# Kernel tuning notes

Hardware: AMD Instinct MI355X
Metric: run time of the kernel (lower is better)

Reference implementation:

```python
import jax, jax.numpy as jnp
import numpy as np

D_MODEL = 2048
D_INNER = 4096            # expand * d_model
D_XB = 1024
D_STATE = 128
HEADDIM = 64
NHEADS = D_INNER // HEADDIM            # 64
NGROUPS = D_INNER // D_STATE           # 32 (d_inner == ngroups * d_state)
HPG = NHEADS // NGROUPS                # heads per B/C group = 2
REPEAT = D_INNER // D_XB               # repeat_kv factor = 4
XB_GROUPS = D_XB // D_STATE            # 8
CHUNK = 256
D_CONV = 4
CONV_DIM = D_INNER + 2 * D_XB          # 6144
D_IN_PROJ = D_INNER + 2 * D_XB + D_INNER + NHEADS  # 10304 -> d_mlp = 0
NORM_GS = D_INNER // NGROUPS           # gated group-RMSNorm group size = 128
EPS = 1e-5


def setup_inputs() -> dict:
    key = jax.random.key(0)
    ks = jax.random.split(key, 8)
    u = jax.random.normal(ks[0], (2, 2048, D_MODEL), jnp.float32)
    W_in = jax.random.normal(ks[1], (D_IN_PROJ, D_MODEL), jnp.float32) * 0.02
    conv_w = jax.random.normal(ks[2], (CONV_DIM, D_CONV), jnp.float32) * 0.2
    conv_b = jnp.zeros((CONV_DIM,), jnp.float32)
    # dt_bias = inverse-softplus of dt ~ LogUniform(dt_min, dt_max), as in __init__
    dt = jnp.exp(jax.random.uniform(ks[3], (NHEADS,), jnp.float32)
                 * (np.log(0.1) - np.log(0.001)) + np.log(0.001))
    dt_bias = dt + jnp.log(-jnp.expm1(-dt))
    A_log = jnp.log(jax.random.uniform(ks[4], (NHEADS,), jnp.float32, minval=1.0, maxval=16.0))
    D = jnp.ones((NHEADS,), jnp.float32)
    norm_weight = jnp.ones((D_INNER,), jnp.float32)
    W_out = jax.random.normal(ks[5], (D_MODEL, D_INNER), jnp.float32) * 0.02
    return dict(u=u, W_in=W_in, conv_w=conv_w, conv_b=conv_b, dt_bias=dt_bias,
                A_log=A_log, D=D, norm_weight=norm_weight, W_out=W_out)


def _segsum(x):
    # x: (..., T); out[..., t, s] = sum_{s < i <= t} x_i for s <= t else -inf
    T = x.shape[-1]
    cs = jnp.cumsum(x, axis=-1)
    seg = cs[..., :, None] - cs[..., None, :]
    mask = jnp.tril(jnp.ones((T, T), bool))
    return jnp.where(mask, seg, -jnp.inf)


def _chunked_scan(x, dt, A, Bh, Ch, D):
    # SSD chunked selective scan (mamba_chunk_scan_combined math).
    # x: (b,l,h,p), dt: (b,l,h) post-softplus, A: (h,), Bh/Ch: (b,l,h,n), D: (h,)
    b, l, h, p = x.shape
    c = l // CHUNK
    xc = x.reshape(b, c, CHUNK, h, p)
    dtc = dt.reshape(b, c, CHUNK, h)
    Bc = Bh.reshape(b, c, CHUNK, h, D_STATE)
    Cc = Ch.reshape(b, c, CHUNK, h, D_STATE)
    dA = jnp.transpose(dtc * A, (0, 3, 1, 2))          # (b,h,c,cl)
    dA_cs = jnp.cumsum(dA, axis=-1)                     # (b,h,c,cl)
    L = jnp.exp(_segsum(dA))                            # (b,h,c,cl,cl), lower-tri decay
    xdt = xc * dtc[..., None]                           # (b,c,cl,h,p)
    # intra-chunk (diagonal block) output
    G = jnp.einsum('bclhn,bcshn->bhcls', Cc, Bc)
    Y_diag = jnp.einsum('bhcls,bcshp->bclhp', G * L, xdt)
    # per-chunk final states
    decay_states = jnp.exp(dA_cs[..., -1:] - dA_cs)     # (b,h,c,cl)
    states = jnp.einsum('bcshn,bhcs,bcshp->bchpn', Bc, decay_states, xdt)
    # inter-chunk recurrence
    chunk_decay = jnp.exp(dA_cs[..., -1])               # (b,h,c)
    states_t = jnp.moveaxis(states, 1, 0)               # (c,b,h,p,n)
    decay_t = jnp.moveaxis(chunk_decay, -1, 0)          # (c,b,h)
    def step(carry, inp):
        s, d = inp
        return carry * d[..., None, None] + s, carry
    _, prev = jax.lax.scan(step, jnp.zeros_like(states_t[0]), (states_t, decay_t))
    prev = jnp.moveaxis(prev, 0, 1)                     # (b,c,h,p,n) state entering each chunk
    Y_off = jnp.einsum('bclhn,bchpn,bhcl->bclhp', Cc, prev, jnp.exp(dA_cs))
    y = Y_diag + Y_off + xc * D[:, None]                # D skip uses raw x
    return y.reshape(b, l, h, p)


def reference(u, W_in, conv_w, conv_b, dt_bias, A_log, D, norm_weight, W_out):
    b, l, _ = u.shape
    zxbcdt = u @ W_in.T                                 # (b,l,10304); d_mlp == 0
    z, xBC, dt = jnp.split(zxbcdt, [D_INNER, D_INNER + CONV_DIM], axis=-1)
    # causal depthwise conv1d (kernel D_CONV) + SiLU (causal_conv1d_fn semantics)
    xp = jnp.pad(xBC, ((0, 0), (D_CONV - 1, 0), (0, 0)))
    conv = conv_b
    for k in range(D_CONV):
        conv = conv + xp[:, k:k + l, :] * conv_w[:, k]
    xBC = jax.nn.silu(conv)
    x, B, C = jnp.split(xBC, [D_XB, 2 * D_XB], axis=-1)
    # GQA-style repeat_kv (repeat_interleave over d_state-sized groups)
    x = jnp.repeat(x.reshape(b, l, XB_GROUPS, D_STATE), REPEAT, axis=2).reshape(b, l, D_INNER)
    B = jnp.repeat(B.reshape(b, l, XB_GROUPS, D_STATE), REPEAT, axis=2)   # (b,l,NGROUPS,n)
    C = C.reshape(b, l, NGROUPS, D_STATE)
    # broadcast groups to heads (head h uses group h // HPG)
    Bh = jnp.repeat(B, HPG, axis=2)
    Ch = jnp.repeat(C, HPG, axis=2)
    xh = x.reshape(b, l, NHEADS, HEADDIM)
    dt = jax.nn.softplus(dt + dt_bias)                  # dt_softplus=True
    A = -jnp.exp(A_log)
    y = _chunked_scan(xh, dt, A, Bh, Ch, D).reshape(b, l, D_INNER)
    # RMSNormGated (norm_before_gate=False): gate then grouped RMSNorm
    y = y * jax.nn.silu(z)
    yg = y.reshape(b, l, NGROUPS, NORM_GS)
    rstd = jax.lax.rsqrt(jnp.mean(yg * yg, axis=-1, keepdims=True) + EPS)
    y = (yg * rstd).reshape(b, l, D_INNER) * norm_weight
    return y @ W_out.T
```

## Files before the change

kernel.cpp:

```cpp
#include <hip/hip_runtime.h>
#include <cstdint>
#include <cstddef>

typedef unsigned int uint;
typedef unsigned short ushort;

typedef __bf16 bf16x8 __attribute__((ext_vector_type(8)));
typedef float f32x4 __attribute__((ext_vector_type(4)));

__device__ __forceinline__ float bflo(uint u) { return __uint_as_float(u << 16); }
__device__ __forceinline__ float bfhi(uint u) { return __uint_as_float(u & 0xffff0000u); }
__device__ __forceinline__ float bf2f(ushort s) { return __uint_as_float(((uint)s) << 16); }
__device__ __forceinline__ ushort f2bf(float f) {
    uint u = __float_as_uint(f);
    u += 0x7fffu + ((u >> 16) & 1u);
    return (ushort)(u >> 16);
}
__device__ __forceinline__ uint pk2(float lo, float hi) {
    return (uint)f2bf(lo) | ((uint)f2bf(hi) << 16);
}
__device__ __forceinline__ void unpack8(uint4 v, float* f) {
    f[0] = bflo(v.x); f[1] = bfhi(v.x); f[2] = bflo(v.y); f[3] = bfhi(v.y);
    f[4] = bflo(v.z); f[5] = bfhi(v.z); f[6] = bflo(v.w); f[7] = bfhi(v.w);
}

typedef __attribute__((address_space(1))) const unsigned int* as1_cuptr;
typedef __attribute__((address_space(3))) unsigned int* as3_uptr;
__device__ __forceinline__ void gload_lds16(const void* g, void* l) {
    __builtin_amdgcn_global_load_lds((as1_cuptr)g, (as3_uptr)l, 16, 0, 0);
}

#define LTOT 4096
#define DMODEL 2048
#define DINNER 4096
#define DSTATE 128
#define NHEADS 64
#define CONVDIM 6144
#define DPROJ 10304
#define CHUNK 256
#define NCHUNK 16

__global__ void cvt_all(const float* __restrict__ u, const float* __restrict__ Wi,
                        const float* __restrict__ Wo, ushort* __restrict__ ub,
                        ushort* __restrict__ wib, ushort* __restrict__ wob) {
    int i = blockIdx.x * 256 + threadIdx.x;
    const float* src; ushort* dst; int j;
    if (i < 2097152)      { src = u;  dst = ub;  j = i; }
    else if (i < 7372800) { src = Wi; dst = wib; j = i - 2097152; }
    else if (i < 9469952) { src = Wo; dst = wob; j = i - 7372800; }
    else return;
    float4 v = ((const float4*)src)[j];
    ushort4 o;
    o.x = f2bf(v.x); o.y = f2bf(v.y); o.z = f2bf(v.z); o.w = f2bf(v.w);
    ((ushort4*)dst)[j] = o;
}

#define MFMA_OP __builtin_amdgcn_mfma_f32_16x16x32_bf16
#define MMX(MB, AV, BV) do { \
  _Pragma("unroll") \
  for (int _m = 0; _m < 4; _m++) \
    _Pragma("unroll") \
    for (int _n = 0; _n < 4; _n++) \
      acc[(MB)+_m][_n] = MFMA_OP(AV[_m], BV[_n], acc[(MB)+_m][_n], 0, 0, 0); \
} while (0)

#define RD8(BASE, OFF) (*(const bf16x8*)((BASE) + (OFF)))

__global__ __launch_bounds__(512, 2) void gemm256_in(
    const ushort* __restrict__ X, const ushort* __restrict__ W,
    ushort* __restrict__ zbuf, ushort* __restrict__ xbc, float* __restrict__ dtraw) {
    __shared__ ushort AL[2][16384];
    __shared__ ushort BL[2][16384];
    const int NBN = 41;
    int q = gridDim.x >> 3;
    int wg = blockIdx.x;
    int swz = (wg & 7) * q + (wg >> 3);
    int per = NBN * 4;
    int sg = swz / per, rr = swz % per;
    int bm = sg * 4 + (rr & 3);
    int bn = rr >> 2;
    int tid = threadIdx.x;
    int lane = tid & 63, w = tid >> 6;
    int wr = w >> 2, wc = w & 3;
    int lr = lane & 15, g = lane >> 4;
    int y00 = ((lr >> 1) << 7) | ((lr & 1) << 6) | (g << 4);
    int z00 = y00 ^ (((y00 >> 7) & 7) << 4);
    int aBase = wr * 8192 + z00;
    int bBase = wc * 4096 + z00;
    int z0 = tid * 16, z1 = z0 + 8192;
    int y0 = z0 ^ (((z0 >> 7) & 7) << 4);
    int y1 = z1 ^ (((z1 >> 7) & 7) << 4);
    int row0s = ((y0 >> 7) << 1) | ((y0 >> 6) & 1), kbe0 = (y0 & 63) >> 1;
    int row1s = ((y1 >> 7) << 1) | ((y1 >> 6) & 1), kbe1 = (y1 & 63) >> 1;
    const ushort* gA0 = &X[(size_t)(bm * 256 + row0s) * 2048 + kbe0];
    const ushort* gA1 = &X[(size_t)(bm * 256 + row1s) * 2048 + kbe1];
    const ushort* gB0 = &W[(size_t)(bn * 256 + row0s) * 2048 + kbe0];
    const ushort* gB1 = &W[(size_t)(bn * 256 + row1s) * 2048 + kbe1];
    int wOff = w * 1024;

#define STAGE(DB, ARR, KP, P0, P1, KO) do { \
    gload_lds16((P0) + (KO) + (KP) * 32, (char*)(ARR) + (DB) * 32768 + (KP) * 16384 + wOff); \
    gload_lds16((P1) + (KO) + (KP) * 32, (char*)(ARR) + (DB) * 32768 + (KP) * 16384 + wOff + 8192); \
} while (0)

    f32x4 acc[8][4] = {};
    bf16x8 bLo[4], bHi[4], aE[4], aO[4];
    STAGE(0, AL, 0, gA0, gA1, 0);
    STAGE(0, BL, 0, gB0, gB1, 0);
    STAGE(0, AL, 1, gA0, gA1, 0);
    STAGE(0, BL, 1, gB0, gB1, 0);
    asm volatile("s_waitcnt vmcnt(4)" ::: "memory");
    __builtin_amdgcn_s_barrier();
    __builtin_amdgcn_sched_barrier(0);
    {
        const char* Ab = (const char*)AL;
        const char* Bb = (const char*)BL;
        #pragma unroll
        for (int i = 0; i < 4; i++) {
            bLo[i] = RD8(Bb, bBase + i * 1024);
            aE[i]  = RD8(Ab, aBase + i * 1024);
        }
    }

    for (int t = 0; t < 32; ++t) {
        int buf = t & 1, nb = buf ^ 1;
        int ko = ((t + 1) & 31) * 64;
        const char* Ab  = (const char*)AL + buf * 32768;
        const char* Bb  = (const char*)BL + buf * 32768;
        const char* AbN = (const char*)AL + nb * 32768;
        const char* BbN = (const char*)BL + nb * 32768;
        #pragma unroll
        for (int i = 0; i < 4; i++) aO[i] = RD8(Ab, aBase + 4096 + i * 1024);
        STAGE(nb, AL, 0, gA0, gA1, ko);
        __builtin_amdgcn_s_setprio(1);
        MMX(0, aE, bLo);
        __builtin_amdgcn_s_setprio(0);
        __builtin_amdgcn_sched_barrier(0);
        asm volatile("s_waitcnt vmcnt(2)" ::: "memory");
        __builtin_amdgcn_s_barrier();
        __builtin_amdgcn_sched_barrier(0);
        #pragma unroll
        for (int i = 0; i < 4; i++) {
            bHi[i] = RD8(Bb, bBase + 16384 + i * 1024);
            aE[i]  = RD8(Ab, aBase + 16384 + i * 1024);
        }
        STAGE(nb, BL, 0, gB0, gB1, ko);
        __builtin_amdgcn_s_setprio(1);
        MMX(4, aO, bLo);
        __builtin_amdgcn_s_setprio(0);
        __builtin_amdgcn_sched_barrier(0);
        #pragma unroll
        for (int i = 0; i < 4; i++) aO[i] = RD8(Ab, aBase + 16384 + 4096 + i * 1024);
        STAGE(nb, AL, 1, gA0, gA1, ko);
        __builtin_amdgcn_s_setprio(1);
        MMX(0, aE, bHi);
        __builtin_amdgcn_s_setprio(0);
        __builtin_amdgcn_sched_barrier(0);
        asm volatile("s_waitcnt vmcnt(2)" ::: "memory");
        __builtin_amdgcn_s_barrier();
        __builtin_amdgcn_sched_barrier(0);
        #pragma unroll
        for (int i = 0; i < 4; i++) {
            bLo[i] = RD8(BbN, bBase + i * 1024);
            aE[i]  = RD8(AbN, aBase + i * 1024);
        }
        STAGE(nb, BL, 1, gB0, gB1, ko);
        __builtin_amdgcn_s_setprio(1);
        MMX(4, aO, bHi);
        __builtin_amdgcn_s_setprio(0);
        __builtin_amdgcn_sched_barrier(0);
    }
    asm volatile("s_waitcnt vmcnt(0)" ::: "memory");

    int rq = g * 4;
    #pragma unroll
    for (int mf = 0; mf < 8; mf++) {
        int row0 = bm * 256 + wr * 128 + mf * 16 + rq;
        #pragma unroll
        for (int n = 0; n < 4; n++) {
            int cb0 = bn * 256 + wc * 64 + n * 16;
            int col = cb0 + lr;
            if (cb0 < 4096) {
                #pragma unroll
                for (int r = 0; r < 4; r++)
                    zbuf[(size_t)(row0 + r) * DINNER + col] = f2bf(acc[mf][n][r]);
            } else if (cb0 < 10240) {
                #pragma unroll
                for (int r = 0; r < 4; r++)
                    xbc[(size_t)(row0 + r) * CONVDIM + (col - 4096)] = f2bf(acc[mf][n][r]);
            } else if (cb0 < 10304) {
                #pragma unroll
                for (int r = 0; r < 4; r++)
                    dtraw[(size_t)(row0 + r) * 64 + (col - 10240)] = acc[mf][n][r];
            }
        }
    }
}
#undef STAGE

#define MM8(M0, AV, BV) do { \
  _Pragma("unroll") \
  for (int _m = 0; _m < 2; _m++) \
    _Pragma("unroll") \
    for (int _n = 0; _n < 4; _n++) \
      acc[(M0)+_m][_n] = MFMA_OP(AV[(M0)+_m], BV[_n], acc[(M0)+_m][_n], 0, 0, 0); \
} while (0)

__global__ __launch_bounds__(512, 2) void gemm256_out(
    const ushort* __restrict__ X, const ushort* __restrict__ W,
    float* __restrict__ outF) {
    __shared__ ushort AL[2][16384];
    __shared__ ushort BL[2][8192];
    int q = gridDim.x >> 3;
    int wg = blockIdx.x;
    int swz = (wg & 7) * q + (wg >> 3);
    int per = 16 * 4;
    int sg = swz / per, rr = swz % per;
    int bm = sg * 4 + (rr & 3);
    int bn = rr >> 2;
    int tid = threadIdx.x;
    int lane = tid & 63, w = tid >> 6;
    int wr = w >> 1, wc = w & 1;
    int lr = lane & 15, g = lane >> 4;
    int y00 = ((lr >> 1) << 7) | ((lr & 1) << 6) | (g << 4);
    int z00 = y00 ^ (((y00 >> 7) & 7) << 4);
    int aBase = wr * 4096 + z00;
    int bBase = wc * 4096 + z00;
    int z0 = tid * 16, z1 = z0 + 8192;
    int y0 = z0 ^ (((z0 >> 7) & 7) << 4);
    int y1 = z1 ^ (((z1 >> 7) & 7) << 4);
    int rowA0 = ((y0 >> 7) << 1) | ((y0 >> 6) & 1), kA0 = (y0 & 63) >> 1;
    int rowA1 = ((y1 >> 7) << 1) | ((y1 >> 6) & 1), kA1 = (y1 & 63) >> 1;
    const ushort* gA0 = &X[(size_t)(bm * 256 + rowA0) * 4096 + kA0];
    const ushort* gA1 = &X[(size_t)(bm * 256 + rowA1) * 4096 + kA1];
    const ushort* gB  = &W[(size_t)(bn * 128 + rowA0) * 4096 + kA0];
    int wOff = w * 1024;

#define STAGEA(DB, KP, KO) do { \
    gload_lds16(gA0 + (KO) + (KP) * 32, (char*)AL + (DB) * 32768 + (KP) * 16384 + wOff); \
    gload_lds16(gA1 + (KO) + (KP) * 32, (char*)AL + (DB) * 32768 + (KP) * 16384 + wOff + 8192); \
} while (0)
#define STAGEB(DB, KP, KO) \
    gload_lds16(gB + (KO) + (KP) * 32, (char*)BL + (DB) * 16384 + (KP) * 8192 + wOff)

    f32x4 acc[4][4] = {};
    bf16x8 aP[4], bP[4], aQ[4], bQ[4];
    STAGEA(0, 0, 0); STAGEB(0, 0, 0);
    STAGEA(0, 1, 0); STAGEB(0, 1, 0);
    asm volatile("s_waitcnt vmcnt(3)" ::: "memory");
    __builtin_amdgcn_s_barrier();
    __builtin_amdgcn_sched_barrier(0);
    #pragma unroll
    for (int i = 0; i < 4; i++) {
        bP[i] = RD8((const char*)BL, bBase + i * 1024);
        aP[i] = RD8((const char*)AL, aBase + i * 1024);
    }

    for (int t = 0; t < 64; ++t) {
        int buf = t & 1, nb = buf ^ 1;
        int ko = ((t + 1) & 63) * 64;
        const char* Ab  = (const char*)AL + buf * 32768;
        const char* Bb  = (const char*)BL + buf * 16384;
        const char* AbN = (const char*)AL + nb * 32768;
        const char* BbN = (const char*)BL + nb * 16384;
        STAGEA(nb, 0, ko); STAGEB(nb, 0, ko);
        __builtin_amdgcn_s_setprio(1);
        MM8(0, aP, bP);
        MM8(2, aP, bP);
        __builtin_amdgcn_s_setprio(0);
        __builtin_amdgcn_sched_barrier(0);
        asm volatile("s_waitcnt vmcnt(3)" ::: "memory");
        __builtin_amdgcn_s_barrier();
        __builtin_amdgcn_sched_barrier(0);
        #pragma unroll
        for (int i = 0; i < 4; i++) {
            bQ[i] = RD8(Bb, bBase + 8192 + i * 1024);
            aQ[i] = RD8(Ab, aBase + 16384 + i * 1024);
        }
        STAGEA(nb, 1, ko); STAGEB(nb, 1, ko);
        __builtin_amdgcn_s_setprio(1);
        MM8(0, aQ, bQ);
        __builtin_amdgcn_s_setprio(0);
        __builtin_amdgcn_sched_barrier(0);
        asm volatile("s_waitcnt vmcnt(3)" ::: "memory");
        __builtin_amdgcn_s_barrier();
        __builtin_amdgcn_sched_barrier(0);
        #pragma unroll
        for (int i = 0; i < 4; i++) {
            bP[i] = RD8(BbN, bBase + i * 1024);
            aP[i] = RD8(AbN, aBase + i * 1024);
        }
        __builtin_amdgcn_s_setprio(1);
        MM8(2, aQ, bQ);
        __builtin_amdgcn_s_setprio(0);
        __builtin_amdgcn_sched_barrier(0);
    }
    asm volatile("s_waitcnt vmcnt(0)" ::: "memory");

    int rq = g * 4;
    #pragma unroll
    for (int mf = 0; mf < 4; mf++) {
        int row0 = bm * 256 + wr * 64 + mf * 16 + rq;
        #pragma unroll
        for (int nf = 0; nf < 4; nf++) {
            int col = bn * 128 + wc * 64 + nf * 16 + lr;
            #pragma unroll
            for (int r = 0; r < 4; r++)
                outF[(size_t)(row0 + r) * DMODEL + col] = acc[mf][nf][r];
        }
    }
}
#undef STAGEA
#undef STAGEB

__global__ void conv_kernel(const ushort* __restrict__ xbc, const float* __restrict__ cw,
                            const float* __restrict__ cb, ushort* __restrict__ convout) {
    int c8 = (blockIdx.x * 256 + threadIdx.x) * 8;
    int row0 = blockIdx.y * 4;
    int t0 = row0 & 2047;
    float bias[8];
    {
        float4 b0 = ((const float4*)cb)[c8 / 4];
        float4 b1 = ((const float4*)cb)[c8 / 4 + 1];
        bias[0] = b0.x; bias[1] = b0.y; bias[2] = b0.z; bias[3] = b0.w;
        bias[4] = b1.x; bias[5] = b1.y; bias[6] = b1.z; bias[7] = b1.w;
    }
    float wk[8][4];
    #pragma unroll
    for (int e = 0; e < 8; e++) {
        float4 wv = ((const float4*)cw)[c8 + e];
        wk[e][0] = wv.x; wk[e][1] = wv.y; wk[e][2] = wv.z; wk[e][3] = wv.w;
    }
    float f[7][8];
    #pragma unroll
    for (int j = 0; j < 7; j++) {
        int tt = t0 - 3 + j;
        if (tt >= 0) {
            uint4 v = *(const uint4*)&xbc[(size_t)(row0 - 3 + j) * CONVDIM + c8];
            unpack8(v, f[j]);
        } else {
            #pragma unroll
            for (int e = 0; e < 8; e++) f[j][e] = 0.f;
        }
    }
    #pragma unroll
    for (int r = 0; r < 4; r++) {
        float a[8];
        #pragma unroll
        for (int e = 0; e < 8; e++) {
            a[e] = bias[e];
            #pragma unroll
            for (int k = 0; k < 4; k++) a[e] += f[r + k][e] * wk[e][k];
        }
        uint4 o;
        float s[8];
        #pragma unroll
        for (int e = 0; e < 8; e++) s[e] = a[e] / (1.f + __expf(-a[e]));
        o.x = pk2(s[0], s[1]); o.y = pk2(s[2], s[3]);
        o.z = pk2(s[4], s[5]); o.w = pk2(s[6], s[7]);
        *(uint4*)&convout[(size_t)(row0 + r) * CONVDIM + c8] = o;
    }
}

__global__ void cumsum_kernel(float* __restrict__ dtbuf, const float* __restrict__ dt_bias,
                              const float* __restrict__ A_log, float* __restrict__ dAcs) {
    int bi = blockIdx.x;
    int h = bi & 63, cg = bi >> 6;
    int t = threadIdx.x;
    size_t didx = (size_t)(cg * 256 + t) * 64 + h;
    float x = dtbuf[didx] + dt_bias[h];
    float sp = (x > 20.f) ? x : log1pf(__expf(x));
    dtbuf[didx] = sp;
    float A = -expf(A_log[h]);
    float v = sp * A;
    __shared__ float s[256];
    s[t] = v;
    __syncthreads();
    for (int off = 1; off < 256; off <<= 1) {
        float add = (t >= off) ? s[t - off] : 0.f;
        __syncthreads();
        s[t] += add;
        __syncthreads();
    }
    dAcs[(size_t)bi * 256 + t] = s[t];
}

__global__ __launch_bounds__(256) void states_mfma(
    const ushort* __restrict__ convout, const float* __restrict__ dtsp,
    const float* __restrict__ dAcs, float* __restrict__ states) {
    __shared__ ushort BT[128 * 72];
    __shared__ ushort XT[64 * 72];
    int bi = blockIdx.x;
    int h = bi & 63, cg = bi >> 6;
    int tid = threadIdx.x;
    int rowbase = cg * 256;
    int bcol = 1024 + ((h >> 3) << 7);
    int xcol = ((h >> 3) << 7) + ((h & 1) << 6);
    float dAlast = dAcs[(size_t)bi * 256 + 255];
    int w = tid >> 6, lane = tid & 63, g = lane >> 4, cc = lane & 15;
    f32x4 acc[4][2] = {};
    for (int T = 0; T < 4; T++) {
        __syncthreads();
        int s = lane;
        int srow = rowbase + T * 64 + s;
        #pragma unroll
        for (int i = 0; i < 4; i++) {
            int n0 = (w + i * 4) * 8;
            uint4 v = *(const uint4*)&convout[(size_t)srow * CONVDIM + bcol + n0];
            ushort us[8];
            us[0] = (ushort)v.x; us[1] = (ushort)(v.x >> 16);
            us[2] = (ushort)v.y; us[3] = (ushort)(v.y >> 16);
            us[4] = (ushort)v.z; us[5] = (ushort)(v.z >> 16);
            us[6] = (ushort)v.w; us[7] = (ushort)(v.w >> 16);
            #pragma unroll
            for (int e = 0; e < 8; e++) BT[(n0 + e) * 72 + s] = us[e];
        }
        float wgt = dtsp[(size_t)srow * 64 + h] * __expf(dAlast - dAcs[(size_t)bi * 256 + T * 64 + s]);
        #pragma unroll
        for (int j = 0; j < 2; j++) {
            int p0 = (w * 2 + j) * 8;
            uint4 v = *(const uint4*)&convout[(size_t)srow * CONVDIM + xcol + p0];
            float f[8]; unpack8(v, f);
            #pragma unroll
            for (int e = 0; e < 8; e++) XT[(p0 + e) * 72 + s] = f2bf(f[e] * wgt);
        }
        __syncthreads();
        bf16x8 af[4][2], bw[2][2];
        #pragma unroll
        for (int m = 0; m < 4; m++)
            #pragma unroll
            for (int kb = 0; kb < 2; kb++)
                af[m][kb] = *(const bf16x8*)&XT[(m * 16 + cc) * 72 + kb * 32 + 8 * g];
        #pragma unroll
        for (int np = 0; np < 2; np++)
            #pragma unroll
            for (int kb = 0; kb < 2; kb++)
                bw[np][kb] = *(const bf16x8*)&BT[(w * 32 + np * 16 + cc) * 72 + kb * 32 + 8 * g];
        #pragma unroll
        for (int m = 0; m < 4; m++)
            #pragma unroll
            for (int np = 0; np < 2; np++) {
                acc[m][np] = MFMA_OP(af[m][0], bw[np][0], acc[m][np], 0, 0, 0);
                acc[m][np] = MFMA_OP(af[m][1], bw[np][1], acc[m][np], 0, 0, 0);
            }
    }
    size_t base = (size_t)bi * 8192;
    #pragma unroll
    for (int m = 0; m < 4; m++)
        #pragma unroll
        for (int np = 0; np < 2; np++)
            #pragma unroll
            for (int r = 0; r < 4; r++) {
                int p = m * 16 + 4 * g + r;
                int n = w * 32 + np * 16 + cc;
                states[base + (size_t)p * 128 + n] = acc[m][np][r];
            }
}

__global__ void recur_kernel(const float* __restrict__ dAcs, float* __restrict__ states) {
    int blk = blockIdx.x;
    int pq = blk & 7, bh = blk >> 3;
    int h = bh & 63, b = bh >> 6;
    int tid = threadIdx.x;
    int p = pq * 8 + (tid >> 5);
    int n0 = (tid & 31) * 4;
    float4 carry = make_float4(0.f, 0.f, 0.f, 0.f);
    for (int c = 0; c < 8; c++) {
        int bi = (b * 8 + c) * 64 + h;
        float decay = __expf(dAcs[(size_t)bi * 256 + 255]);
        size_t idx = (size_t)bi * 8192 + (size_t)p * 128 + n0;
        float4 tmp = *(const float4*)&states[idx];
        *(float4*)&states[idx] = carry;
        carry.x = carry.x * decay + tmp.x;
        carry.y = carry.y * decay + tmp.y;
        carry.z = carry.z * decay + tmp.z;
        carry.w = carry.w * decay + tmp.w;
    }
}

__global__ __launch_bounds__(256, 2) void yscan_mfma(
    const ushort* __restrict__ convout, const float* __restrict__ dtsp,
    const float* __restrict__ dAcs, const float* __restrict__ states,
    ushort* __restrict__ y) {
    __shared__ ushort XT[64 * 264];
    __shared__ ushort PR[64 * 136];
    __shared__ ushort PV[4 * 16 * 72];
    __shared__ float sdA[256];
    int bi = blockIdx.x;
    int h = bi & 63, cg = bi >> 6;
    int tid = threadIdx.x;
    int rowbase = cg * 256;
    int bcol = 1024 + ((h >> 3) << 7);
    int ccol = 2048 + ((h >> 1) << 7);
    int xcol = ((h >> 3) << 7) + ((h & 1) << 6);

    sdA[tid] = dAcs[(size_t)bi * 256 + tid];
    #pragma unroll
    for (int i = 0; i < 4; i++) {
        int s = i * 64 + (tid & 63);
        float dtv = dtsp[(size_t)(rowbase + s) * 64 + h];
        #pragma unroll
        for (int j = 0; j < 2; j++) {
            int p0 = (((tid >> 6) << 1) + j) << 3;
            uint4 v = *(const uint4*)&convout[(size_t)(rowbase + s) * CONVDIM + xcol + p0];
            float f[8]; unpack8(v, f);
            #pragma unroll
            for (int e = 0; e < 8; e++) XT[(p0 + e) * 264 + s] = f2bf(f[e] * dtv);
        }
    }
    {
        const float* pv = &states[(size_t)bi * 8192];
        #pragma unroll
        for (int i = 0; i < 8; i++) {
            int flat = i * 1024 + tid * 4;
            float4 v = *(const float4*)&pv[flat];
            int p = flat >> 7, n = flat & 127;
            *(uint*)&PR[p * 136 + n]     = pk2(v.x, v.y);
            *(uint*)&PR[p * 136 + n + 2] = pk2(v.z, v.w);
        }
    }
    __syncthreads();

    int w = tid >> 6, lane = tid & 63, g = lane >> 4, c = lane & 15;
    int wbase = w * 64;
    const ushort* Crow0 = &convout[(size_t)(rowbase + wbase + c) * CONVDIM + ccol + 8 * g];

    f32x4 yac[4][4] = {};
    #pragma unroll
    for (int kb = 0; kb < 4; kb++) {
        bf16x8 pb[4];
        #pragma unroll
        for (int np = 0; np < 4; np++)
            pb[np] = *(const bf16x8*)&PR[(16 * np + c) * 136 + kb * 32 + 8 * g];
        #pragma unroll
        for (int m = 0; m < 4; m++) {
            bf16x8 cf = *(const bf16x8*)&Crow0[(size_t)(m * 16) * CONVDIM + kb * 32];
            #pragma unroll
            for (int np = 0; np < 4; np++)
                yac[m][np] = MFMA_OP(cf, pb[np], yac[m][np], 0, 0, 0);
        }
    }
    float al[4][4];
    float Sw = sdA[wbase];
    float eSw = __expf(Sw);
    #pragma unroll
    for (int m = 0; m < 4; m++)
        #pragma unroll
        for (int r = 0; r < 4; r++) {
            float dAl = sdA[wbase + m * 16 + 4 * g + r];
            al[m][r] = __expf(dAl - Sw);
            float el = al[m][r] * eSw;
            #pragma unroll
            for (int np = 0; np < 4; np++) yac[m][np][r] *= el;
        }

    ushort* pvs = &PV[w * 1152];
    for (int T = 0; T <= w; T++) {
        f32x4 sac[4][4] = {};
        #pragma unroll
        for (int kb = 0; kb < 4; kb++) {
            bf16x8 bb[4];
            #pragma unroll
            for (int np = 0; np < 4; np++)
                bb[np] = *(const bf16x8*)&convout[(size_t)(rowbase + T * 64 + 16 * np + c) * CONVDIM + bcol + kb * 32 + 8 * g];
            #pragma unroll
            for (int m = 0; m < 4; m++) {
                bf16x8 cf = *(const bf16x8*)&Crow0[(size_t)(m * 16) * CONVDIM + kb * 32];
                #pragma unroll
                for (int np = 0; np < 4; np++)
                    sac[m][np] = MFMA_OP(cf, bb[np], sac[m][np], 0, 0, 0);
            }
        }
        bf16x8 xb[4][2];
        #pragma unroll
        for (int np = 0; np < 4; np++)
            #pragma unroll
            for (int k2 = 0; k2 < 2; k2++)
                xb[np][k2] = *(const bf16x8*)&XT[(16 * np + c) * 264 + T * 64 + k2 * 32 + 8 * g];
        if (T < w) {
            float ET = sdA[T * 64 + 63];
            float cT = __expf(Sw - ET);
            float bc[4];
            #pragma unroll
            for (int np = 0; np < 4; np++)
                bc[np] = __expf(ET - sdA[T * 64 + 16 * np + c]) * cT;
            #pragma unroll
            for (int m = 0; m < 4; m++) {
                #pragma unroll
                for (int np = 0; np < 4; np++) {
                    float s0 = bc[np];
                    #pragma unroll
                    for (int r = 0; r < 4; r++)
                        pvs[(4 * g + r) * 72 + 16 * np + c] = f2bf(sac[m][np][r] * (al[m][r] * s0));
                }
                bf16x8 pa0 = *(const bf16x8*)&pvs[c * 72 + 8 * g];
                bf16x8 pa1 = *(const bf16x8*)&pvs[c * 72 + 32 + 8 * g];
                #pragma unroll
                for (int np = 0; np < 4; np++) {
                    yac[m][np] = MFMA_OP(pa0, xb[np][0], yac[m][np], 0, 0, 0);
                    yac[m][np] = MFMA_OP(pa1, xb[np][1], yac[m][np], 0, 0, 0);
                }
            }
        } else {
            #pragma unroll
            for (int m = 0; m < 4; m++) {
                float dal[4];
                #pragma unroll
                for (int r = 0; r < 4; r++) dal[r] = sdA[wbase + m * 16 + 4 * g + r];
                #pragma unroll
                for (int np = 0; np < 4; np++) {
                    int s_loc = w * 64 + 16 * np + c;
                    float dAs = sdA[s_loc];
                    #pragma unroll
                    for (int r = 0; r < 4; r++) {
                        int l_loc = wbase + m * 16 + 4 * g + r;
                        float v = (s_loc <= l_loc) ? sac[m][np][r] * __expf(dal[r] - dAs) : 0.f;
                        pvs[(4 * g + r) * 72 + 16 * np + c] = f2bf(v);
                    }
                }
                bf16x8 pa0 = *(const bf16x8*)&pvs[c * 72 + 8 * g];
                bf16x8 pa1 = *(const bf16x8*)&pvs[c * 72 + 32 + 8 * g];
                #pragma unroll
                for (int np = 0; np < 4; np++) {
                    yac[m][np] = MFMA_OP(pa0, xb[np][0], yac[m][np], 0, 0, 0);
                    yac[m][np] = MFMA_OP(pa1, xb[np][1], yac[m][np], 0, 0, 0);
                }
            }
        }
    }
    #pragma unroll
    for (int m = 0; m < 4; m++)
        #pragma unroll
        for (int np = 0; np < 4; np++)
            #pragma unroll
            for (int r = 0; r < 4; r++) {
                int l = wbase + m * 16 + 4 * g + r;
                y[(size_t)(rowbase + l) * DINNER + h * 64 + 16 * np + c] = f2bf(yac[m][np][r]);
            }
}

__global__ void norm_kernel(ushort* __restrict__ y, const ushort* __restrict__ zbuf,
                            const ushort* __restrict__ convout, const float* __restrict__ Dvec,
                            const float* __restrict__ nw) {
    int row = blockIdx.x;
    int g = blockIdx.y * 4 + (threadIdx.x >> 6);
    int lane = threadIdx.x & 63;
    int cbase = g * 128 + lane * 2;
    int h = cbase >> 6;
    int p = cbase & 63;
    int xc = ((h >> 3) << 7) + ((h & 1) << 6) + p;
    uint yv = *(const uint*)&y[(size_t)row * DINNER + cbase];
    uint zv = *(const uint*)&zbuf[(size_t)row * DINNER + cbase];
    uint xv = *(const uint*)&convout[(size_t)row * CONVDIM + xc];
    float Dh = Dvec[h];
    float y0 = bflo(yv) + Dh * bflo(xv), y1 = bfhi(yv) + Dh * bfhi(xv);
    float z0 = bflo(zv), z1 = bfhi(zv);
    float v0 = y0 * (z0 / (1.f + __expf(-z0)));
    float v1 = y1 * (z1 / (1.f + __expf(-z1)));
    float ss = v0 * v0 + v1 * v1;
    #pragma unroll
    for (int off = 32; off; off >>= 1) ss += __shfl_xor(ss, off, 64);
    float rstd = rsqrtf(ss * (1.f / 128.f) + 1e-5f);
    v0 *= rstd * nw[cbase];
    v1 *= rstd * nw[cbase + 1];
    *(uint*)&y[(size_t)row * DINNER + cbase] = pk2(v0, v1);
}

extern "C" void kernel_launch(void* const* d_in, const int* in_sizes, int n_in,
                              void* d_out, int out_size, void* d_ws, size_t ws_size,
                              hipStream_t stream) {
    const float* u       = (const float*)d_in[0];
    const float* W_in    = (const float*)d_in[1];
    const float* conv_w  = (const float*)d_in[2];
    const float* conv_b  = (const float*)d_in[3];
    const float* dt_bias = (const float*)d_in[4];
    const float* A_log   = (const float*)d_in[5];
    const float* Dvec    = (const float*)d_in[6];
    const float* nw      = (const float*)d_in[7];
    const float* W_out   = (const float*)d_in[8];

    char* ws = (char*)d_ws;
    size_t off = 0;
    auto alloc = [&](size_t bytes) { void* p = ws + off; off += (bytes + 255) & ~(size_t)255; return p; };
    ushort* zbuf    = (ushort*)alloc((size_t)LTOT * DINNER * 2);
    void*   shreg   = alloc((size_t)LTOT * CONVDIM * 2);
    ushort* xbc     = (ushort*)shreg;
    float*  states  = (float*)shreg;
    float*  dtbuf   = (float*) alloc((size_t)LTOT * 64 * 4);
    void*   convreg = alloc((size_t)LTOT * CONVDIM * 2);
    ushort* Win_bf  = (ushort*)convreg;
    ushort* convout = (ushort*)convreg;
    float*  dAcs    = (float*) alloc((size_t)1024 * 256 * 4);
    void*   ybreg   = alloc((size_t)LTOT * DINNER * 2);
    ushort* u_bf    = (ushort*)ybreg;
    ushort* ybuf    = (ushort*)ybreg;
    ushort* Wout_bf = (ushort*)alloc((size_t)DMODEL * DINNER * 2);

    cvt_all<<<dim3(36992), dim3(256), 0, stream>>>(u, W_in, W_out, u_bf, Win_bf, Wout_bf);
    gemm256_in<<<dim3(656), dim3(512), 0, stream>>>(u_bf, Win_bf, zbuf, xbc, dtbuf);
    conv_kernel<<<dim3(3, 1024), dim3(256), 0, stream>>>(xbc, conv_w, conv_b, convout);
    cumsum_kernel<<<dim3(1024), dim3(256), 0, stream>>>(dtbuf, dt_bias, A_log, dAcs);
    states_mfma<<<dim3(1024), dim3(256), 0, stream>>>(convout, dtbuf, dAcs, states);
    recur_kernel<<<dim3(1024), dim3(256), 0, stream>>>(dAcs, states);
    yscan_mfma<<<dim3(1024), dim3(256), 0, stream>>>(convout, dtbuf, dAcs, states, ybuf);
    norm_kernel<<<dim3(4096, 8), dim3(256), 0, stream>>>(ybuf, zbuf, convout, Dvec, nw);
    gemm256_out<<<dim3(256), dim3(512), 0, stream>>>(ybuf, Wout_bf, (float*)d_out);
}
```

Measured before the change: 458.7 us.

## Shrink input-projection GEMM M tile to 128 and double grid size

The input projection GEMM moves from 256x256 tiles to 128x256 tiles. This halves the A-side LDS buffer and the accumulator count, and the grid doubles from 656 to 1312 workgroups. The pipeline is rebuilt with new stage macros, waitcnt values and MFMA grouping. The aim is better CU occupancy and load balance on the 256-CU part, at the cost of lower arithmetic intensity and B tiles being reloaded twice as often.

After: 497.4 us. +8.4%, slower.

```diff
diff --git a/kernel.cpp b/kernel.cpp
--- a/kernel.cpp
+++ b/kernel.cpp
@@ -56,20 +56,19 @@
 }
 
 #define MFMA_OP __builtin_amdgcn_mfma_f32_16x16x32_bf16
-#define MMX(MB, AV, BV) do { \
+#define RD8(BASE, OFF) (*(const bf16x8*)((BASE) + (OFF)))
+#define MM8(M0, AV, BV) do { \
   _Pragma("unroll") \
-  for (int _m = 0; _m < 4; _m++) \
+  for (int _m = 0; _m < 2; _m++) \
     _Pragma("unroll") \
     for (int _n = 0; _n < 4; _n++) \
-      acc[(MB)+_m][_n] = MFMA_OP(AV[_m], BV[_n], acc[(MB)+_m][_n], 0, 0, 0); \
+      acc[(M0)+_m][_n] = MFMA_OP(AV[(M0)+_m], BV[_n], acc[(M0)+_m][_n], 0, 0, 0); \
 } while (0)
 
-#define RD8(BASE, OFF) (*(const bf16x8*)((BASE) + (OFF)))
-
-__global__ __launch_bounds__(512, 2) void gemm256_in(
+__global__ __launch_bounds__(512, 2) void gemm_in(
     const ushort* __restrict__ X, const ushort* __restrict__ W,
     ushort* __restrict__ zbuf, ushort* __restrict__ xbc, float* __restrict__ dtraw) {
-    __shared__ ushort AL[2][16384];
+    __shared__ ushort AL[2][8192];
     __shared__ ushort BL[2][16384];
     const int NBN = 41;
     int q = gridDim.x >> 3;
@@ -85,126 +84,105 @@
     int lr = lane & 15, g = lane >> 4;
     int y00 = ((lr >> 1) << 7) | ((lr & 1) << 6) | (g << 4);
     int z00 = y00 ^ (((y00 >> 7) & 7) << 4);
-    int aBase = wr * 8192 + z00;
+    int aBase = wr * 4096 + z00;
     int bBase = wc * 4096 + z00;
     int z0 = tid * 16, z1 = z0 + 8192;
     int y0 = z0 ^ (((z0 >> 7) & 7) << 4);
     int y1 = z1 ^ (((z1 >> 7) & 7) << 4);
     int row0s = ((y0 >> 7) << 1) | ((y0 >> 6) & 1), kbe0 = (y0 & 63) >> 1;
     int row1s = ((y1 >> 7) << 1) | ((y1 >> 6) & 1), kbe1 = (y1 & 63) >> 1;
-    const ushort* gA0 = &X[(size_t)(bm * 256 + row0s) * 2048 + kbe0];
-    const ushort* gA1 = &X[(size_t)(bm * 256 + row1s) * 2048 + kbe1];
+    const ushort* gA  = &X[(size_t)(bm * 128 + row0s) * 2048 + kbe0];
     const ushort* gB0 = &W[(size_t)(bn * 256 + row0s) * 2048 + kbe0];
     const ushort* gB1 = &W[(size_t)(bn * 256 + row1s) * 2048 + kbe1];
     int wOff = w * 1024;
 
-#define STAGE(DB, ARR, KP, P0, P1, KO) do { \
-    gload_lds16((P0) + (KO) + (KP) * 32, (char*)(ARR) + (DB) * 32768 + (KP) * 16384 + wOff); \
-    gload_lds16((P1) + (KO) + (KP) * 32, (char*)(ARR) + (DB) * 32768 + (KP) * 16384 + wOff + 8192); \
+#define STAGEA(DB, KP, KO) \
+    gload_lds16(gA + (KO) + (KP) * 32, (char*)AL + (DB) * 16384 + (KP) * 8192 + wOff)
+#define STAGEB(DB, KP, KO) do { \
+    gload_lds16(gB0 + (KO) + (KP) * 32, (char*)BL + (DB) * 32768 + (KP) * 16384 + wOff); \
+    gload_lds16(gB1 + (KO) + (KP) * 32, (char*)BL + (DB) * 32768 + (KP) * 16384 + wOff + 8192); \
 } while (0)
 
-    f32x4 acc[8][4] = {};
-    bf16x8 bLo[4], bHi[4], aE[4], aO[4];
-    STAGE(0, AL, 0, gA0, gA1, 0);
-    STAGE(0, BL, 0, gB0, gB1, 0);
-    STAGE(0, AL, 1, gA0, gA1, 0);
-    STAGE(0, BL, 1, gB0, gB1, 0);
-    asm volatile("s_waitcnt vmcnt(4)" ::: "memory");
+    f32x4 acc[4][4] = {};
+    bf16x8 aP[4], bP[4], aQ[4], bQ[4];
+    STAGEA(0, 0, 0); STAGEB(0, 0, 0);
+    STAGEA(0, 1, 0); STAGEB(0, 1, 0);
+    asm volatile("s_waitcnt vmcnt(3)" ::: "memory");
     __builtin_amdgcn_s_barrier();
     __builtin_amdgcn_sched_barrier(0);
-    {
-        const char* Ab = (const char*)AL;
-        const char* Bb = (const char*)BL;
-        #pragma unroll
-        for (int i = 0; i < 4; i++) {
-            bLo[i] = RD8(Bb, bBase + i * 1024);
-            aE[i]  = RD8(Ab, aBase + i * 1024);
-        }
+    #pragma unroll
+    for (int i = 0; i < 4; i++) {
+        bP[i] = RD8((const char*)BL, bBase + i * 1024);
+        aP[i] = RD8((const char*)AL, aBase + i * 1024);
     }
 
     for (int t = 0; t < 32; ++t) {
         int buf = t & 1, nb = buf ^ 1;
         int ko = ((t + 1) & 31) * 64;
-        const char* Ab  = (const char*)AL + buf * 32768;
+        const char* Ab  = (const char*)AL + buf * 16384;
         const char* Bb  = (const char*)BL + buf * 32768;
-        const char* AbN = (const char*)AL + nb * 32768;
+        const char* AbN = (const char*)AL + nb * 16384;
         const char* BbN = (const char*)BL + nb * 32768;
-        #pragma unroll
-        for (int i = 0; i < 4; i++) aO[i] = RD8(Ab, aBase + 4096 + i * 1024);
-        STAGE(nb, AL, 0, gA0, gA1, ko);
+        STAGEA(nb, 0, ko); STAGEB(nb, 0, ko);
         __builtin_amdgcn_s_setprio(1);
-        MMX(0, aE, bLo);
+        MM8(0, aP, bP);
+        MM8(2, aP, bP);
         __builtin_amdgcn_s_setprio(0);
         __builtin_amdgcn_sched_barrier(0);
-        asm volatile("s_waitcnt vmcnt(2)" ::: "memory");
+        asm volatile("s_waitcnt vmcnt(3)" ::: "memory");
         __builtin_amdgcn_s_barrier();
         __builtin_amdgcn_sched_barrier(0);
         #pragma unroll
         for (int i = 0; i < 4; i++) {
-            bHi[i] = RD8(Bb, bBase + 16384 + i * 1024);
-            aE[i]  = RD8(Ab, aBase + 16384 + i * 1024);
-        }
-        STAGE(nb, BL, 0, gB0, gB1, ko);
+            bQ[i] = RD8(Bb, bBase + 16384 + i * 1024);
+            aQ[i] = RD8(Ab, aBase + 8192 + i * 1024);
+        }
+        STAGEA(nb, 1, ko); STAGEB(nb, 1, ko);
         __builtin_amdgcn_s_setprio(1);
-        MMX(4, aO, bLo);
+        MM8(0, aQ, bQ);
         __builtin_amdgcn_s_setprio(0);
         __builtin_amdgcn_sched_barrier(0);
-        #pragma unroll
-        for (int i = 0; i < 4; i++) aO[i] = RD8(Ab, aBase + 16384 + 4096 + i * 1024);
-        STAGE(nb, AL, 1, gA0, gA1, ko);
+        asm volatile("s_waitcnt vmcnt(3)" ::: "memory");
+        __builtin_amdgcn_s_barrier();
+        __builtin_amdgcn_sched_barrier(0);
+        #pragma unroll
+        for (int i = 0; i < 4; i++) {
+            bP[i] = RD8(BbN, bBase + i * 1024);
+            aP[i] = RD8(AbN, aBase + i * 1024);
+        }
         __builtin_amdgcn_s_setprio(1);
-        MMX(0, aE, bHi);
+        MM8(2, aQ, bQ);
         __builtin_amdgcn_s_setprio(0);
         __builtin_amdgcn_sched_barrier(0);
-        asm volatile("s_waitcnt vmcnt(2)" ::: "memory");
-        __builtin_amdgcn_s_barrier();
-        __builtin_amdgcn_sched_barrier(0);
-        #pragma unroll
-        for (int i = 0; i < 4; i++) {
-            bLo[i] = RD8(BbN, bBase + i * 1024);
-            aE[i]  = RD8(AbN, aBase + i * 1024);
-        }
-        STAGE(nb, BL, 1, gB0, gB1, ko);
-        __builtin_amdgcn_s_setprio(1);
-        MMX(4, aO, bHi);
-        __builtin_amdgcn_s_setprio(0);
-        __builtin_amdgcn_sched_barrier(0);
     }
     asm volatile("s_waitcnt vmcnt(0)" ::: "memory");
 
     int rq = g * 4;
     #pragma unroll
-    for (int mf = 0; mf < 8; mf++) {
-        int row0 = bm * 256 + wr * 128 + mf * 16 + rq;
-        #pragma unroll
-        for (int n = 0; n < 4; n++) {
-            int cb0 = bn * 256 + wc * 64 + n * 16;
+    for (int mf = 0; mf < 4; mf++) {
+        int row0 = bm * 128 + wr * 64 + mf * 16 + rq;
+        #pragma unroll
+        for (int nf = 0; nf < 4; nf++) {
+            int cb0 = bn * 256 + wc * 64 + nf * 16;
             int col = cb0 + lr;
             if (cb0 < 4096) {
                 #pragma unroll
                 for (int r = 0; r < 4; r++)
-                    zbuf[(size_t)(row0 + r) * DINNER + col] = f2bf(acc[mf][n][r]);
+                    zbuf[(size_t)(row0 + r) * DINNER + col] = f2bf(acc[mf][nf][r]);
             } else if (cb0 < 10240) {
                 #pragma unroll
                 for (int r = 0; r < 4; r++)
-                    xbc[(size_t)(row0 + r) * CONVDIM + (col - 4096)] = f2bf(acc[mf][n][r]);
+                    xbc[(size_t)(row0 + r) * CONVDIM + (col - 4096)] = f2bf(acc[mf][nf][r]);
             } else if (cb0 < 10304) {
                 #pragma unroll
                 for (int r = 0; r < 4; r++)
-                    dtraw[(size_t)(row0 + r) * 64 + (col - 10240)] = acc[mf][n][r];
+                    dtraw[(size_t)(row0 + r) * 64 + (col - 10240)] = acc[mf][nf][r];
             }
         }
     }
 }
-#undef STAGE
-
-#define MM8(M0, AV, BV) do { \
-  _Pragma("unroll") \
-  for (int _m = 0; _m < 2; _m++) \
-    _Pragma("unroll") \
-    for (int _n = 0; _n < 4; _n++) \
-      acc[(M0)+_m][_n] = MFMA_OP(AV[(M0)+_m], BV[_n], acc[(M0)+_m][_n], 0, 0, 0); \
-} while (0)
+#undef STAGEA
+#undef STAGEB
 
 __global__ __launch_bounds__(512, 2) void gemm256_out(
     const ushort* __restrict__ X, const ushort* __restrict__ W,
@@ -697,7 +675,7 @@
     ushort* Wout_bf = (ushort*)alloc((size_t)DMODEL * DINNER * 2);
 
     cvt_all<<<dim3(36992), dim3(256), 0, stream>>>(u, W_in, W_out, u_bf, Win_bf, Wout_bf);
-    gemm256_in<<<dim3(656), dim3(512), 0, stream>>>(u_bf, Win_bf, zbuf, xbc, dtbuf);
+    gemm_in<<<dim3(1312), dim3(512), 0, stream>>>(u_bf, Win_bf, zbuf, xbc, dtbuf);
     conv_kernel<<<dim3(3, 1024), dim3(256), 0, stream>>>(xbc, conv_w, conv_b, convout);
     cumsum_kernel<<<dim3(1024), dim3(256), 0, stream>>>(dtbuf, dt_bias, A_log, dAcs);
     states_mfma<<<dim3(1024), dim3(256), 0, stream>>>(convout, dtbuf, dAcs, states);
```

## Interleave chunk rows across warps to balance causal intra-chunk work

Applied to the files above, without the earlier changes.

Each warp now owns rows m*64 + w*16 across all four 64-row sub-blocks, instead of one contiguous 64-row block. Before, the causal triangle gave warp w a share of work proportional to w+1. With interleaving every warp does the same amount, and B tiles for each T are loaded once and reused across m. The cost is more live registers (bbT holds 16 bf16x8 values), which may lower occupancy or cause spills.

After: 459.0 us. No clear change (+0.1%).

```diff
diff --git a/kernel.cpp b/kernel.cpp
--- a/kernel.cpp
+++ b/kernel.cpp
@@ -522,8 +522,7 @@
     __syncthreads();
 
     int w = tid >> 6, lane = tid & 63, g = lane >> 4, c = lane & 15;
-    int wbase = w * 64;
-    const ushort* Crow0 = &convout[(size_t)(rowbase + wbase + c) * CONVDIM + ccol + 8 * g];
+    const ushort* Crow0 = &convout[(size_t)(rowbase + w * 16 + c) * CONVDIM + ccol + 8 * g];
 
     f32x4 yac[4][4] = {};
     #pragma unroll
@@ -534,98 +533,86 @@
             pb[np] = *(const bf16x8*)&PR[(16 * np + c) * 136 + kb * 32 + 8 * g];
         #pragma unroll
         for (int m = 0; m < 4; m++) {
-            bf16x8 cf = *(const bf16x8*)&Crow0[(size_t)(m * 16) * CONVDIM + kb * 32];
+            bf16x8 cf = *(const bf16x8*)&Crow0[(size_t)(m * 64) * CONVDIM + kb * 32];
             #pragma unroll
             for (int np = 0; np < 4; np++)
                 yac[m][np] = MFMA_OP(cf, pb[np], yac[m][np], 0, 0, 0);
         }
     }
     float al[4][4];
-    float Sw = sdA[wbase];
-    float eSw = __expf(Sw);
-    #pragma unroll
-    for (int m = 0; m < 4; m++)
+    #pragma unroll
+    for (int m = 0; m < 4; m++) {
+        float Sm = sdA[m * 64];
+        float eSm = __expf(Sm);
         #pragma unroll
         for (int r = 0; r < 4; r++) {
-            float dAl = sdA[wbase + m * 16 + 4 * g + r];
-            al[m][r] = __expf(dAl - Sw);
-            float el = al[m][r] * eSw;
+            float dAl = sdA[m * 64 + w * 16 + 4 * g + r];
+            al[m][r] = __expf(dAl - Sm);
+            float el = al[m][r] * eSm;
             #pragma unroll
             for (int np = 0; np < 4; np++) yac[m][np][r] *= el;
         }
+    }
 
     ushort* pvs = &PV[w * 1152];
-    for (int T = 0; T <= w; T++) {
-        f32x4 sac[4][4] = {};
-        #pragma unroll
-        for (int kb = 0; kb < 4; kb++) {
-            bf16x8 bb[4];
+    #pragma unroll
+    for (int T = 0; T < 4; T++) {
+        bf16x8 bbT[4][4];
+        #pragma unroll
+        for (int kb = 0; kb < 4; kb++)
             #pragma unroll
             for (int np = 0; np < 4; np++)
-                bb[np] = *(const bf16x8*)&convout[(size_t)(rowbase + T * 64 + 16 * np + c) * CONVDIM + bcol + kb * 32 + 8 * g];
-            #pragma unroll
-            for (int m = 0; m < 4; m++) {
-                bf16x8 cf = *(const bf16x8*)&Crow0[(size_t)(m * 16) * CONVDIM + kb * 32];
+                bbT[kb][np] = *(const bf16x8*)&convout[(size_t)(rowbase + T * 64 + 16 * np + c) * CONVDIM + bcol + kb * 32 + 8 * g];
+        bf16x8 xb[4][2];
+        #pragma unroll
+        for (int np = 0; np < 4; np++)
+            #pragma unroll
+            for (int k2 = 0; k2 < 2; k2++)
+                xb[np][k2] = *(const bf16x8*)&XT[(16 * np + c) * 264 + T * 64 + k2 * 32 + 8 * g];
+        float ET = sdA[T * 64 + 63];
+        #pragma unroll
+        for (int m = 0; m < 4; m++) {
+            if (m < T) continue;
+            f32x4 sac[4] = {};
+            #pragma unroll
+            for (int kb = 0; kb < 4; kb++) {
+                bf16x8 cf = *(const bf16x8*)&Crow0[(size_t)(m * 64) * CONVDIM + kb * 32];
                 #pragma unroll
                 for (int np = 0; np < 4; np++)
-                    sac[m][np] = MFMA_OP(cf, bb[np], sac[m][np], 0, 0, 0);
+                    sac[np] = MFMA_OP(cf, bbT[kb][np], sac[np], 0, 0, 0);
             }
-        }
-        bf16x8 xb[4][2];
-        #pragma unroll
-        for (int np = 0; np < 4; np++)
-            #pragma unroll
-            for (int k2 = 0; k2 < 2; k2++)
-                xb[np][k2] = *(const bf16x8*)&XT[(16 * np + c) * 264 + T * 64 + k2 * 32 + 8 * g];
-        if (T < w) {
-            float ET = sdA[T * 64 + 63];
-            float cT = __expf(Sw - ET);
-            float bc[4];
-            #pragma unroll
-            for (int np = 0; np < 4; np++)
-                bc[np] = __expf(ET - sdA[T * 64 + 16 * np + c]) * cT;
-            #pragma unroll
-            for (int m = 0; m < 4; m++) {
+            if (m > T) {
+                float cTm = __expf(sdA[m * 64] - ET);
                 #pragma unroll
                 for (int np = 0; np < 4; np++) {
-                    float s0 = bc[np];
+                    float bcv = __expf(ET - sdA[T * 64 + 16 * np + c]) * cTm;
                     #pragma unroll
                     for (int r = 0; r < 4; r++)
-                        pvs[(4 * g + r) * 72 + 16 * np + c] = f2bf(sac[m][np][r] * (al[m][r] * s0));
+                        pvs[(4 * g + r) * 72 + 16 * np + c] = f2bf(sac[np][r] * (al[m][r] * bcv));
                 }
-                bf16x8 pa0 = *(const bf16x8*)&pvs[c * 72 + 8 * g];
-                bf16x8 pa1 = *(const bf16x8*)&pvs[c * 72 + 32 + 8 * g];
+            } else {
+                float dal[4];
+                #pragma unroll
+                for (int r = 0; r < 4; r++) dal[r] = sdA[m * 64 + w * 16 + 4 * g + r];
                 #pragma unroll
                 for (int np = 0; np < 4; np++) {
-                    yac[m][np] = MFMA_OP(pa0, xb[np][0], yac[m][np], 0, 0, 0);
-                    yac[m][np] = MFMA_OP(pa1, xb[np][1], yac[m][np], 0, 0, 0);
-                }
-            }
-        } else {
-            #pragma unroll
-            for (int m = 0; m < 4; m++) {
-                float dal[4];
-                #pragma unroll
-                for (int r = 0; r < 4; r++) dal[r] = sdA[wbase + m * 16 + 4 * g + r];
-                #pragma unroll
-                for (int np = 0; np < 4; np++) {
-                    int s_loc = w * 64 + 16 * np + c;
+                    int s_loc = m * 64 + 16 * np + c;
                     float dAs = sdA[s_loc];
                     #pragma unroll
                     for (int r = 0; r < 4; r++) {
-                        int l_loc = wbase + m * 16 + 4 * g + r;
-                        float v = (s_loc <= l_loc) ? sac[m][np][r] * __expf(dal[r] - dAs) : 0.f;
+                        int l_loc = m * 64 + w * 16 + 4 * g + r;
+                        float v = (s_loc <= l_loc) ? sac[np][r] * __expf(dal[r] - dAs) : 0.f;
                         pvs[(4 * g + r) * 72 + 16 * np + c] = f2bf(v);
                     }
                 }
-                bf16x8 pa0 = *(const bf16x8*)&pvs[c * 72 + 8 * g];
-                bf16x8 pa1 = *(const bf16x8*)&pvs[c * 72 + 32 + 8 * g];
-                #pragma unroll
-                for (int np = 0; np < 4; np++) {
-                    yac[m][np] = MFMA_OP(pa0, xb[np][0], yac[m][np], 0, 0, 0);
-                    yac[m][np] = MFMA_OP(pa1, xb[np][1], yac[m][np], 0, 0, 0);
-                }
             }
+            bf16x8 pa0 = *(const bf16x8*)&pvs[c * 72 + 8 * g];
+            bf16x8 pa1 = *(const bf16x8*)&pvs[c * 72 + 32 + 8 * g];
+            #pragma unroll
+            for (int np = 0; np < 4; np++) {
+                yac[m][np] = MFMA_OP(pa0, xb[np][0], yac[m][np], 0, 0, 0);
+                yac[m][np] = MFMA_OP(pa1, xb[np][1], yac[m][np], 0, 0, 0);
+            }
         }
     }
     #pragma unroll
@@ -634,7 +621,7 @@
         for (int np = 0; np < 4; np++)
             #pragma unroll
             for (int r = 0; r < 4; r++) {
-                int l = wbase + m * 16 + 4 * g + r;
+                int l = m * 64 + w * 16 + 4 * g + r;
                 y[(size_t)(rowbase + l) * DINNER + h * 64 + 16 * np + c] = f2bf(yac[m][np][r]);
             }
 }
```
